# Performance work log

Measured on AMD Instinct MI355X. Metric: run time of the kernel, lower is better.

Reference implementation:

```python
import jax, jax.numpy as jnp
import numpy as np

N = 4096
RANK = 4
B = 2048
DT = 1.0
TAU = 1.0
ALPHA = float(np.sqrt(np.pi) / 2.0)  # erf slope so phi'(0)=1


def setup_inputs() -> dict:
    key = jax.random.key(0)
    k1, k2, k3, k4, k5, k6 = jax.random.split(key, 6)
    return {
        "x_t": jax.random.normal(k1, (1, B), dtype=jnp.float32),
        "h": jax.random.normal(k2, (N, B), dtype=jnp.float32),
        "m": jax.random.normal(k3, (N, 1), dtype=jnp.float32),
        "u": jax.random.normal(k4, (N, RANK), dtype=jnp.float32),
        "v": jax.random.normal(k5, (N, RANK), dtype=jnp.float32),
        "z": jax.random.normal(k6, (N, 1), dtype=jnp.float32),
    }


def reference(x_t, h, m, u, v, z):
    # phi(h) = erf(alpha * h)
    phi_h = jax.lax.erf(ALPHA * h)                      # [N, B]
    # W @ phi_h with W = (1/N) u v^T, reassociated to exploit low rank
    # (mathematically identical to materializing W)
    wph = (u @ (v.T @ phi_h)) / N                       # [N, B]
    h_update = wph + m @ x_t                            # [N, B]
    h_new = h + (DT / TAU) * (-h + h_update)            # [N, B]
    y = (z.T @ phi_h) / N                               # [1, B]
    return (y, h_new)
```

## Files before the change

### kernel.cpp

```cpp
#include <hip/hip_runtime.h>
#include <math.h>

#define N 4096
#define B 2048
#define RANK 4
#define ALPHA 0.8862269254527580f
#define INV_N (1.0f / 4096.0f)

#define SPLITS 256
#define RPB (N / SPLITS)
#define R3 16

__global__ __launch_bounds__(256) void k_reduce_partial(
    const float* __restrict__ h, const float* __restrict__ v,
    const float* __restrict__ z, float* __restrict__ partials) {
  __shared__ float lv[RPB * RANK];
  __shared__ float lz[RPB];
  const int tid = threadIdx.x;
  const int b4 = blockIdx.x * 1024 + tid * 4;
  const int row0 = blockIdx.y * RPB;

  if (tid < RPB * RANK) lv[tid] = v[row0 * RANK + tid];
  if (tid >= 64 && tid < 64 + RPB) lz[tid - 64] = z[row0 + (tid - 64)];
  __syncthreads();

  float4 a0 = {0.f, 0.f, 0.f, 0.f}, a1 = a0, a2 = a0, a3 = a0, az = a0;
  const float* hp = h + (size_t)row0 * B + b4;
#pragma unroll
  for (int i = 0; i < RPB; ++i) {
    const float4 hv = *(const float4*)(hp + (size_t)i * B);
    float4 p;
    p.x = erff(ALPHA * hv.x);
    p.y = erff(ALPHA * hv.y);
    p.z = erff(ALPHA * hv.z);
    p.w = erff(ALPHA * hv.w);
    const float v0 = lv[i * 4 + 0], v1 = lv[i * 4 + 1];
    const float v2 = lv[i * 4 + 2], v3 = lv[i * 4 + 3];
    const float zi = lz[i];
    a0.x = fmaf(v0, p.x, a0.x); a0.y = fmaf(v0, p.y, a0.y);
    a0.z = fmaf(v0, p.z, a0.z); a0.w = fmaf(v0, p.w, a0.w);
    a1.x = fmaf(v1, p.x, a1.x); a1.y = fmaf(v1, p.y, a1.y);
    a1.z = fmaf(v1, p.z, a1.z); a1.w = fmaf(v1, p.w, a1.w);
    a2.x = fmaf(v2, p.x, a2.x); a2.y = fmaf(v2, p.y, a2.y);
    a2.z = fmaf(v2, p.z, a2.z); a2.w = fmaf(v2, p.w, a2.w);
    a3.x = fmaf(v3, p.x, a3.x); a3.y = fmaf(v3, p.y, a3.y);
    a3.z = fmaf(v3, p.z, a3.z); a3.w = fmaf(v3, p.w, a3.w);
    az.x = fmaf(zi, p.x, az.x); az.y = fmaf(zi, p.y, az.y);
    az.z = fmaf(zi, p.z, az.z); az.w = fmaf(zi, p.w, az.w);
  }

  float* pp = partials + (size_t)blockIdx.y * 5 * B + b4;
  *(float4*)(pp + 0 * B) = a0;
  *(float4*)(pp + 1 * B) = a1;
  *(float4*)(pp + 2 * B) = a2;
  *(float4*)(pp + 3 * B) = a3;
  *(float4*)(pp + 4 * B) = az;
}

__global__ __launch_bounds__(256) void k_reduce_final(
    const float* __restrict__ partials, float* __restrict__ sfin,
    float* __restrict__ y) {
  const int o = blockIdx.x * 256 + threadIdx.x;
  const int r = o / B;
  const int b = o - r * B;
  float s = 0.f;
#pragma unroll 16
  for (int sp = 0; sp < SPLITS; ++sp)
    s += partials[((size_t)sp * 5 + r) * B + b];
  if (r < RANK)
    sfin[(size_t)r * B + b] = s;
  else
    y[b] = s * INV_N;
}

__global__ __launch_bounds__(256) void k_update(
    const float* __restrict__ sfin, const float* __restrict__ u,
    const float* __restrict__ m, const float* __restrict__ x,
    float* __restrict__ hnew) {
  const int b4 = (blockIdx.x * 256 + threadIdx.x) * 4;
  const int row0 = blockIdx.y * R3;

  const float4 s0 = *(const float4*)(sfin + 0 * B + b4);
  const float4 s1 = *(const float4*)(sfin + 1 * B + b4);
  const float4 s2 = *(const float4*)(sfin + 2 * B + b4);
  const float4 s3 = *(const float4*)(sfin + 3 * B + b4);
  const float4 xv = *(const float4*)(x + b4);

#pragma unroll
  for (int i = 0; i < R3; ++i) {
    const int n = row0 + i;
    const float4 uv = *(const float4*)(u + (size_t)n * RANK);
    const float mv = m[n];
    float4 o;
    o.x = fmaf(mv, xv.x,
               (s0.x * uv.x + s1.x * uv.y + s2.x * uv.z + s3.x * uv.w) * INV_N);
    o.y = fmaf(mv, xv.y,
               (s0.y * uv.x + s1.y * uv.y + s2.y * uv.z + s3.y * uv.w) * INV_N);
    o.z = fmaf(mv, xv.z,
               (s0.z * uv.x + s1.z * uv.y + s2.z * uv.z + s3.z * uv.w) * INV_N);
    o.w = fmaf(mv, xv.w,
               (s0.w * uv.x + s1.w * uv.y + s2.w * uv.z + s3.w * uv.w) * INV_N);
    *(float4*)(hnew + (size_t)n * B + b4) = o;
  }
}

extern "C" void kernel_launch(void* const* d_in, const int* in_sizes, int n_in,
                              void* d_out, int out_size, void* d_ws,
                              size_t ws_size, hipStream_t stream) {
  const float* x = (const float*)d_in[0];
  const float* h = (const float*)d_in[1];
  const float* m = (const float*)d_in[2];
  const float* u = (const float*)d_in[3];
  const float* v = (const float*)d_in[4];
  const float* z = (const float*)d_in[5];

  float* y = (float*)d_out;
  float* hnew = (float*)d_out + B;

  float* partials = (float*)d_ws;
  float* sfin = (float*)d_ws + (size_t)SPLITS * 5 * B;

  k_reduce_partial<<<dim3(B / 1024, SPLITS), 256, 0, stream>>>(h, v, z,
                                                               partials);
  k_reduce_final<<<(5 * B) / 256, 256, 0, stream>>>(partials, sfin, y);
  k_update<<<dim3(B / 1024, N / R3), 256, 0, stream>>>(sfin, u, m, x, hnew);
}
```

Before: 123.6 us.

## Fuse three kernels into one cooperative kernel with grid-wide syncs

Replaces the partial-reduce, final-reduce and update kernels with a single cooperative launch of 256 blocks of 512 threads, separated by grid.sync barriers. The final reduction now uses 160 blocks, each splitting the partial sum across 8 thread groups with a shared-memory combine. Loads of h and stores of hnew use nontemporal hints. This removes two kernel launch gaps and spreads the final reduction over more threads, at the cost of grid-barrier overhead and a fixed grid of 256 blocks, one per compute unit, that leaves occupancy low in the streaming phases.

```diff
diff --git a/kernel.cpp b/kernel.cpp
--- a/kernel.cpp
+++ b/kernel.cpp
@@ -1,5 +1,8 @@
 #include <hip/hip_runtime.h>
+#include <hip/hip_cooperative_groups.h>
 #include <math.h>
+
+namespace cg = cooperative_groups;
 
 #define N 4096
 #define B 2048
@@ -7,100 +10,125 @@
 #define ALPHA 0.8862269254527580f
 #define INV_N (1.0f / 4096.0f)
 
-#define SPLITS 256
-#define RPB (N / SPLITS)
-#define R3 16
+#define NBLK 256
+#define NTHR 512
+#define RPB (N / NBLK)
+#define P (5 * B)
+#define STRIPE 64
+#define NSTRIPE (P / STRIPE)
+#define GRP 8
+#define SPG (NBLK / GRP)
 
-__global__ __launch_bounds__(256) void k_reduce_partial(
-    const float* __restrict__ h, const float* __restrict__ v,
-    const float* __restrict__ z, float* __restrict__ partials) {
-  __shared__ float lv[RPB * RANK];
-  __shared__ float lz[RPB];
+typedef float vf4 __attribute__((ext_vector_type(4)));
+
+__global__ void __launch_bounds__(NTHR) k_fused(
+    const float* __restrict__ x, const float* __restrict__ h,
+    const float* __restrict__ m, const float* __restrict__ u,
+    const float* __restrict__ v, const float* __restrict__ z,
+    float* __restrict__ y, float* __restrict__ hnew,
+    float* __restrict__ partials, float* __restrict__ sfin) {
+  cg::grid_group grid = cg::this_grid();
   const int tid = threadIdx.x;
-  const int b4 = blockIdx.x * 1024 + tid * 4;
-  const int row0 = blockIdx.y * RPB;
+  const int bid = blockIdx.x;
 
-  if (tid < RPB * RANK) lv[tid] = v[row0 * RANK + tid];
-  if (tid >= 64 && tid < 64 + RPB) lz[tid - 64] = z[row0 + (tid - 64)];
-  __syncthreads();
+  {
+    __shared__ float lv[RPB * RANK];
+    __shared__ float lz[RPB];
+    const int row0 = bid * RPB;
+    if (tid < RPB * RANK) {
+      lv[tid] = v[row0 * RANK + tid];
+    } else if (tid < RPB * RANK + RPB) {
+      lz[tid - RPB * RANK] = z[row0 + (tid - RPB * RANK)];
+    }
+    __syncthreads();
 
-  float4 a0 = {0.f, 0.f, 0.f, 0.f}, a1 = a0, a2 = a0, a3 = a0, az = a0;
-  const float* hp = h + (size_t)row0 * B + b4;
+    vf4 a0 = {0.f, 0.f, 0.f, 0.f};
+    vf4 a1 = a0, a2 = a0, a3 = a0, a4 = a0;
+    const float* hp = h + (size_t)row0 * B + tid * 4;
 #pragma unroll
-  for (int i = 0; i < RPB; ++i) {
-    const float4 hv = *(const float4*)(hp + (size_t)i * B);
-    float4 p;
-    p.x = erff(ALPHA * hv.x);
-    p.y = erff(ALPHA * hv.y);
-    p.z = erff(ALPHA * hv.z);
-    p.w = erff(ALPHA * hv.w);
-    const float v0 = lv[i * 4 + 0], v1 = lv[i * 4 + 1];
-    const float v2 = lv[i * 4 + 2], v3 = lv[i * 4 + 3];
-    const float zi = lz[i];
-    a0.x = fmaf(v0, p.x, a0.x); a0.y = fmaf(v0, p.y, a0.y);
-    a0.z = fmaf(v0, p.z, a0.z); a0.w = fmaf(v0, p.w, a0.w);
-    a1.x = fmaf(v1, p.x, a1.x); a1.y = fmaf(v1, p.y, a1.y);
-    a1.z = fmaf(v1, p.z, a1.z); a1.w = fmaf(v1, p.w, a1.w);
-    a2.x = fmaf(v2, p.x, a2.x); a2.y = fmaf(v2, p.y, a2.y);
-    a2.z = fmaf(v2, p.z, a2.z); a2.w = fmaf(v2, p.w, a2.w);
-    a3.x = fmaf(v3, p.x, a3.x); a3.y = fmaf(v3, p.y, a3.y);
-    a3.z = fmaf(v3, p.z, a3.z); a3.w = fmaf(v3, p.w, a3.w);
-    az.x = fmaf(zi, p.x, az.x); az.y = fmaf(zi, p.y, az.y);
-    az.z = fmaf(zi, p.z, az.z); az.w = fmaf(zi, p.w, az.w);
+    for (int r = 0; r < RPB; ++r) {
+      const vf4 hv =
+          __builtin_nontemporal_load((const vf4*)(hp + (size_t)r * B));
+      vf4 p;
+      p.x = erff(ALPHA * hv.x);
+      p.y = erff(ALPHA * hv.y);
+      p.z = erff(ALPHA * hv.z);
+      p.w = erff(ALPHA * hv.w);
+      const float v0 = lv[r * 4 + 0], v1 = lv[r * 4 + 1];
+      const float v2 = lv[r * 4 + 2], v3 = lv[r * 4 + 3];
+      const float zr = lz[r];
+      a0.x = fmaf(v0, p.x, a0.x); a0.y = fmaf(v0, p.y, a0.y);
+      a0.z = fmaf(v0, p.z, a0.z); a0.w = fmaf(v0, p.w, a0.w);
+      a1.x = fmaf(v1, p.x, a1.x); a1.y = fmaf(v1, p.y, a1.y);
+      a1.z = fmaf(v1, p.z, a1.z); a1.w = fmaf(v1, p.w, a1.w);
+      a2.x = fmaf(v2, p.x, a2.x); a2.y = fmaf(v2, p.y, a2.y);
+      a2.z = fmaf(v2, p.z, a2.z); a2.w = fmaf(v2, p.w, a2.w);
+      a3.x = fmaf(v3, p.x, a3.x); a3.y = fmaf(v3, p.y, a3.y);
+      a3.z = fmaf(v3, p.z, a3.z); a3.w = fmaf(v3, p.w, a3.w);
+      a4.x = fmaf(zr, p.x, a4.x); a4.y = fmaf(zr, p.y, a4.y);
+      a4.z = fmaf(zr, p.z, a4.z); a4.w = fmaf(zr, p.w, a4.w);
+    }
+    float* pp = partials + (size_t)bid * P + tid * 4;
+    *(vf4*)(pp + 0 * B) = a0;
+    *(vf4*)(pp + 1 * B) = a1;
+    *(vf4*)(pp + 2 * B) = a2;
+    *(vf4*)(pp + 3 * B) = a3;
+    *(vf4*)(pp + 4 * B) = a4;
   }
 
-  float* pp = partials + (size_t)blockIdx.y * 5 * B + b4;
-  *(float4*)(pp + 0 * B) = a0;
-  *(float4*)(pp + 1 * B) = a1;
-  *(float4*)(pp + 2 * B) = a2;
-  *(float4*)(pp + 3 * B) = a3;
-  *(float4*)(pp + 4 * B) = az;
-}
+  grid.sync();
 
-__global__ __launch_bounds__(256) void k_reduce_final(
-    const float* __restrict__ partials, float* __restrict__ sfin,
-    float* __restrict__ y) {
-  const int o = blockIdx.x * 256 + threadIdx.x;
-  const int r = o / B;
-  const int b = o - r * B;
-  float s = 0.f;
-#pragma unroll 16
-  for (int sp = 0; sp < SPLITS; ++sp)
-    s += partials[((size_t)sp * 5 + r) * B + b];
-  if (r < RANK)
-    sfin[(size_t)r * B + b] = s;
-  else
-    y[b] = s * INV_N;
-}
+  if (bid < NSTRIPE) {
+    __shared__ float red[GRP][STRIPE];
+    const int c = tid & (STRIPE - 1);
+    const int g = tid >> 6;
+    const float* pp = partials + (size_t)(g * SPG) * P + bid * STRIPE + c;
+    float ssum = 0.f;
+#pragma unroll 8
+    for (int sp = 0; sp < SPG; ++sp)
+      ssum += pp[(size_t)sp * P];
+    red[g][c] = ssum;
+    __syncthreads();
+    if (tid < STRIPE) {
+      float tot = 0.f;
+#pragma unroll
+      for (int g2 = 0; g2 < GRP; ++g2)
+        tot += red[g2][tid];
+      const int f = bid * STRIPE + tid;
+      if (f < RANK * B)
+        sfin[f] = tot;
+      else
+        y[f - RANK * B] = tot * INV_N;
+    }
+  }
 
-__global__ __launch_bounds__(256) void k_update(
-    const float* __restrict__ sfin, const float* __restrict__ u,
-    const float* __restrict__ m, const float* __restrict__ x,
-    float* __restrict__ hnew) {
-  const int b4 = (blockIdx.x * 256 + threadIdx.x) * 4;
-  const int row0 = blockIdx.y * R3;
+  grid.sync();
 
-  const float4 s0 = *(const float4*)(sfin + 0 * B + b4);
-  const float4 s1 = *(const float4*)(sfin + 1 * B + b4);
-  const float4 s2 = *(const float4*)(sfin + 2 * B + b4);
-  const float4 s3 = *(const float4*)(sfin + 3 * B + b4);
-  const float4 xv = *(const float4*)(x + b4);
-
+  {
+    const int row0 = bid * RPB;
+    const int c0 = tid * 4;
+    const vf4 s0 = *(const vf4*)(sfin + 0 * B + c0);
+    const vf4 s1 = *(const vf4*)(sfin + 1 * B + c0);
+    const vf4 s2 = *(const vf4*)(sfin + 2 * B + c0);
+    const vf4 s3 = *(const vf4*)(sfin + 3 * B + c0);
+    const vf4 xv = *(const vf4*)(x + c0);
+    float* op = hnew + (size_t)row0 * B + c0;
 #pragma unroll
-  for (int i = 0; i < R3; ++i) {
-    const int n = row0 + i;
-    const float4 uv = *(const float4*)(u + (size_t)n * RANK);
-    const float mv = m[n];
-    float4 o;
-    o.x = fmaf(mv, xv.x,
-               (s0.x * uv.x + s1.x * uv.y + s2.x * uv.z + s3.x * uv.w) * INV_N);
-    o.y = fmaf(mv, xv.y,
-               (s0.y * uv.x + s1.y * uv.y + s2.y * uv.z + s3.y * uv.w) * INV_N);
-    o.z = fmaf(mv, xv.z,
-               (s0.z * uv.x + s1.z * uv.y + s2.z * uv.z + s3.z * uv.w) * INV_N);
-    o.w = fmaf(mv, xv.w,
-               (s0.w * uv.x + s1.w * uv.y + s2.w * uv.z + s3.w * uv.w) * INV_N);
-    *(float4*)(hnew + (size_t)n * B + b4) = o;
+    for (int i = 0; i < RPB; ++i) {
+      const int n = row0 + i;
+      const vf4 uv = *(const vf4*)(u + (size_t)n * RANK);
+      const float mv = m[n];
+      vf4 o;
+      o.x = fmaf(mv, xv.x,
+                 (s0.x * uv.x + s1.x * uv.y + s2.x * uv.z + s3.x * uv.w) * INV_N);
+      o.y = fmaf(mv, xv.y,
+                 (s0.y * uv.x + s1.y * uv.y + s2.y * uv.z + s3.y * uv.w) * INV_N);
+      o.z = fmaf(mv, xv.z,
+                 (s0.z * uv.x + s1.z * uv.y + s2.z * uv.z + s3.z * uv.w) * INV_N);
+      o.w = fmaf(mv, xv.w,
+                 (s0.w * uv.x + s1.w * uv.y + s2.w * uv.z + s3.w * uv.w) * INV_N);
+      __builtin_nontemporal_store(o, (vf4*)(op + (size_t)i * B));
+    }
   }
 }
 
@@ -118,10 +146,11 @@
   float* hnew = (float*)d_out + B;
 
   float* partials = (float*)d_ws;
-  float* sfin = (float*)d_ws + (size_t)SPLITS * 5 * B;
+  float* sfin = partials + (size_t)NBLK * P;
 
-  k_reduce_partial<<<dim3(B / 1024, SPLITS), 256, 0, stream>>>(h, v, z,
-                                                               partials);
-  k_reduce_final<<<(5 * B) / 256, 256, 0, stream>>>(partials, sfin, y);
-  k_update<<<dim3(B / 1024, N / R3), 256, 0, stream>>>(sfin, u, m, x, hnew);
+  void* args[] = {(void*)&x, (void*)&h, (void*)&m,    (void*)&u,
+                  (void*)&v, (void*)&z, (void*)&y,    (void*)&hnew,
+                  (void*)&partials, (void*)&sfin};
+  hipLaunchCooperativeKernel((const void*)k_fused, dim3(NBLK), dim3(NTHR),
+                             args, 0, stream);
 }
```

Measured after the change: 187.4 us. 1.52x slower.
